# Kernel optimization log

Hardware: AMD Instinct MI355X
Metric: run time of the kernel (lower is better)

Reference implementation:

```python
import jax, jax.numpy as jnp
import numpy as np

H, DH = 8, 64            # heads, dim_head (module defaults)
B, N, DN, DE = 1, 512, 128, 64  # batch, nodes, node feat, edge feat
INNER = H * DH


def _w(key, fan_in, fan_out):
    return jax.random.normal(key, (fan_in, fan_out), jnp.float32) / np.sqrt(fan_in)


def setup_inputs() -> dict:
    key = jax.random.key(0)
    ks = jax.random.split(key, 8)
    return {
        "nodes": jax.random.normal(ks[0], (B, N, DN), jnp.float32),
        "edges": jax.random.normal(ks[1], (B, N, N, DE), jnp.float32),
        "mask": jnp.ones((B, N), dtype=bool),
        "Wq": _w(ks[2], DN, INNER), "bq": jnp.zeros((INNER,), jnp.float32),
        "Wk": _w(ks[3], DN, INNER), "bk": jnp.zeros((INNER,), jnp.float32),
        "Wv": _w(ks[4], DN, INNER), "bv": jnp.zeros((INNER,), jnp.float32),
        "We": _w(ks[5], DE, INNER), "be": jnp.zeros((INNER,), jnp.float32),
        "Wo": _w(ks[6], INNER, DN), "bo": jnp.zeros((DN,), jnp.float32),
    }


def _split_heads(x):
    # (b, ..., h*d) -> (b*h, ..., d), matching rearrange 'b ... (h d) -> (b h) ... d'
    b = x.shape[0]
    mid = x.shape[1:-1]
    x = x.reshape(b, *mid, H, DH)
    x = jnp.moveaxis(x, -2, 1)              # (b, h, ..., d)
    return x.reshape(b * H, *mid, DH)


def reference(nodes, edges, mask, Wq, bq, Wk, bk, Wv, bv, We, be, Wo, bo):
    scale = DH ** (-0.5)
    q = _split_heads(nodes @ Wq + bq)        # (bh, n, d)
    k = _split_heads(nodes @ Wk + bk)        # (bh, n, d)
    v = _split_heads(nodes @ Wv + bv)        # (bh, n, d)
    e = _split_heads(edges @ We + be)        # (bh, n, n, d) -- ek == ev == e_kv
    k = k[:, None, :, :] + e                 # (bh, i, j, d) per-ij keys
    v = v[:, None, :, :] + e                 # (bh, i, j, d) per-ij values
    sim = jnp.einsum('bid,bijd->bij', q, k) * scale
    m = mask[:, :, None] & mask[:, None, :]  # (b, i, j)
    m = jnp.repeat(m, H, axis=0)             # (bh, i, j)
    sim = jnp.where(m, sim, -jnp.finfo(sim.dtype).max)
    attn = jax.nn.softmax(sim, axis=-1)
    out = jnp.einsum('bij,bijd->bid', attn, v)           # (bh, n, d)
    out = out.reshape(B, H, N, DH).transpose(0, 2, 1, 3).reshape(B, N, INNER)
    return out @ Wo + bo                                  # (b, n, d_node)
```

## Files before the change

kernel.cpp:

```cpp
#include <hip/hip_runtime.h>
#include <hip/hip_bf16.h>

#define NN 512
#define DNODE 128
#define DEDGE 64
#define NH 8
#define DHD 64
#define DIN 512
#define SCALE 0.125f
#define ESTR 66

typedef unsigned short u16;
typedef unsigned int u32;

__device__ __forceinline__ float bf2f(u16 b) {
    u32 u = ((u32)b) << 16;
    return __builtin_bit_cast(float, u);
}
__device__ __forceinline__ u16 f2bf(float f) {
    u32 u = __builtin_bit_cast(u32, f);
    return (u16)((u + 0x7fffu + ((u >> 16) & 1u)) >> 16);
}

__global__ __launch_bounds__(256) void k_qkv(
    const float* __restrict__ nodes,
    const float* __restrict__ Wq, const float* __restrict__ bq,
    const float* __restrict__ Wk, const float* __restrict__ bk,
    const float* __restrict__ Wv, const float* __restrict__ bv,
    float* __restrict__ Qo, float* __restrict__ Ko, float* __restrict__ Vo)
{
    const int it = blockIdx.x, ct = blockIdx.y, which = blockIdx.z;
    const float* W    = which == 0 ? Wq : (which == 1 ? Wk : Wv);
    const float* bias = which == 0 ? bq : (which == 1 ? bk : bv);
    float* O          = which == 0 ? Qo : (which == 1 ? Ko : Vo);
    __shared__ float As[64][132];
    __shared__ float Bs[128][68];
    const int t = threadIdx.x;
    const int ibase = it * 64, cbase = ct * 64;
#pragma unroll
    for (int p = 0; p < 8; ++p) {
        int r = p * 8 + (t >> 5), c4 = (t & 31) * 4;
        *(float4*)&As[r][c4] = *(const float4*)(nodes + (ibase + r) * DNODE + c4);
    }
#pragma unroll
    for (int p = 0; p < 8; ++p) {
        int k = p * 16 + (t >> 4), c4 = (t & 15) * 4;
        *(float4*)&Bs[k][c4] = *(const float4*)(W + k * DIN + cbase + c4);
    }
    __syncthreads();
    const int tx = t & 15, ty = t >> 4;
    float acc[4][4] = {};
    for (int k = 0; k < DNODE; ++k) {
        float4 b4 = *(const float4*)&Bs[k][tx * 4];
#pragma unroll
        for (int e = 0; e < 4; ++e) {
            float a = As[ty * 4 + e][k];
            acc[e][0] += a * b4.x; acc[e][1] += a * b4.y;
            acc[e][2] += a * b4.z; acc[e][3] += a * b4.w;
        }
    }
    const int h = ct;
#pragma unroll
    for (int ii = 0; ii < 4; ++ii) {
        int i = ibase + ty * 4 + ii;
        float4 o;
        o.x = acc[ii][0] + bias[cbase + tx * 4 + 0];
        o.y = acc[ii][1] + bias[cbase + tx * 4 + 1];
        o.z = acc[ii][2] + bias[cbase + tx * 4 + 2];
        o.w = acc[ii][3] + bias[cbase + tx * 4 + 3];
        *(float4*)(O + ((size_t)h * NN + i) * DHD + tx * 4) = o;
    }
}

__global__ __launch_bounds__(256) void k_qe(
    const float* __restrict__ Q, const float* __restrict__ We, float* __restrict__ QE)
{
    const int it = blockIdx.x, h = blockIdx.y;
    __shared__ float Qs[64][68];
    __shared__ float WsT[64][68];
    const int t = threadIdx.x;
    const int ibase = it * 64;
#pragma unroll
    for (int p = 0; p < 4; ++p) {
        int r = p * 16 + (t >> 4), d4 = (t & 15) * 4;
        *(float4*)&Qs[r][d4] = *(const float4*)(Q + ((size_t)h * NN + ibase + r) * DHD + d4);
    }
#pragma unroll
    for (int p = 0; p < 4; ++p) {
        int c = p * 16 + (t >> 4), d4 = (t & 15) * 4;
        float4 v = *(const float4*)(We + c * DIN + h * DHD + d4);
        WsT[d4 + 0][c] = v.x; WsT[d4 + 1][c] = v.y;
        WsT[d4 + 2][c] = v.z; WsT[d4 + 3][c] = v.w;
    }
    __syncthreads();
    const int tx = t & 15, ty = t >> 4;
    float acc[4][4] = {};
    for (int d = 0; d < DHD; ++d) {
        float4 b4 = *(const float4*)&WsT[d][tx * 4];
#pragma unroll
        for (int e = 0; e < 4; ++e) {
            float a = Qs[ty * 4 + e][d];
            acc[e][0] += a * b4.x; acc[e][1] += a * b4.y;
            acc[e][2] += a * b4.z; acc[e][3] += a * b4.w;
        }
    }
#pragma unroll
    for (int ii = 0; ii < 4; ++ii) {
        int i = ibase + ty * 4 + ii;
        float4 o;
        o.x = SCALE * acc[ii][0]; o.y = SCALE * acc[ii][1];
        o.z = SCALE * acc[ii][2]; o.w = SCALE * acc[ii][3];
        *(float4*)(QE + ((size_t)h * NN + i) * DEDGE + tx * 4) = o;
    }
}

__global__ __launch_bounds__(256) void k_qk(
    const float* __restrict__ Q, const float* __restrict__ K, float* __restrict__ QK)
{
    const int jt = blockIdx.x, it = blockIdx.y, h = blockIdx.z;
    __shared__ float Qs[64][68];
    __shared__ float KsT[64][68];
    const int t = threadIdx.x;
    const int ibase = it * 64, jbase = jt * 64;
#pragma unroll
    for (int p = 0; p < 4; ++p) {
        int r = p * 16 + (t >> 4), d4 = (t & 15) * 4;
        *(float4*)&Qs[r][d4] = *(const float4*)(Q + ((size_t)h * NN + ibase + r) * DHD + d4);
    }
#pragma unroll
    for (int p = 0; p < 4; ++p) {
        int j = p * 16 + (t >> 4), d4 = (t & 15) * 4;
        float4 v = *(const float4*)(K + ((size_t)h * NN + jbase + j) * DHD + d4);
        KsT[d4 + 0][j] = v.x; KsT[d4 + 1][j] = v.y;
        KsT[d4 + 2][j] = v.z; KsT[d4 + 3][j] = v.w;
    }
    __syncthreads();
    const int tx = t & 15, ty = t >> 4;
    float acc[4][4] = {};
    for (int d = 0; d < DHD; ++d) {
        float4 b4 = *(const float4*)&KsT[d][tx * 4];
#pragma unroll
        for (int e = 0; e < 4; ++e) {
            float a = Qs[ty * 4 + e][d];
            acc[e][0] += a * b4.x; acc[e][1] += a * b4.y;
            acc[e][2] += a * b4.z; acc[e][3] += a * b4.w;
        }
    }
#pragma unroll
    for (int ii = 0; ii < 4; ++ii) {
        int i = ibase + ty * 4 + ii;
        float4 o;
        o.x = SCALE * acc[ii][0]; o.y = SCALE * acc[ii][1];
        o.z = SCALE * acc[ii][2]; o.w = SCALE * acc[ii][3];
        *(float4*)(QK + ((size_t)h * NN + i) * NN + jbase + tx * 4) = o;
    }
}

__global__ __launch_bounds__(512, 2) void k_fused(
    const float* __restrict__ edges, const float* __restrict__ QK,
    const float* __restrict__ QE, float* __restrict__ AE, u16* __restrict__ P)
{
    __shared__ u16 erow[NN * ESTR];
    __shared__ u16 Pl[NH][NN];
    __shared__ float qes[NH][DEDGE];
    const int i = blockIdx.x;
    const int t = threadIdx.x;
    const int lane = t & 63, w = t >> 6;

    qes[w][lane] = QE[((size_t)w * NN + i) * DEDGE + lane];

    const float* E = edges + (size_t)i * NN * DEDGE;
#pragma unroll
    for (int p = 0; p < 16; ++p) {
        int idx = p * 2048 + t * 4;
        float4 v = *(const float4*)(E + idx);
        int j = idx >> 6, c = idx & 63;
        u16* dst = &erow[j * ESTR + c];
        *(u32*)(dst)     = ((u32)f2bf(v.x)) | (((u32)f2bf(v.y)) << 16);
        *(u32*)(dst + 2) = ((u32)f2bf(v.z)) | (((u32)f2bf(v.w)) << 16);
    }
    __syncthreads();

    float sim[8];
    const float* qk = QK + ((size_t)w * NN + i) * NN;
#pragma unroll
    for (int r = 0; r < 8; ++r) {
        int j = r * 64 + lane;
        const u16* er = erow + j * ESTR;
        float acc = 0.f;
#pragma unroll
        for (int c = 0; c < 64; c += 4) {
            float4 q4 = *(const float4*)&qes[w][c];
            u32 lo = *(const u32*)(er + c);
            u32 hi = *(const u32*)(er + c + 2);
            acc += q4.x * bf2f((u16)(lo & 0xffff)) + q4.y * bf2f((u16)(lo >> 16))
                 + q4.z * bf2f((u16)(hi & 0xffff)) + q4.w * bf2f((u16)(hi >> 16));
        }
        sim[r] = qk[j] + acc;
    }

    float m = sim[0];
#pragma unroll
    for (int r = 1; r < 8; ++r) m = fmaxf(m, sim[r]);
#pragma unroll
    for (int s = 32; s >= 1; s >>= 1) m = fmaxf(m, __shfl_xor(m, s, 64));
    float p[8], l = 0.f;
#pragma unroll
    for (int r = 0; r < 8; ++r) { p[r] = __expf(sim[r] - m); l += p[r]; }
#pragma unroll
    for (int s = 32; s >= 1; s >>= 1) l += __shfl_xor(l, s, 64);
    float inv = 1.f / l;
    u16* Pg = P + ((size_t)w * NN + i) * NN;
#pragma unroll
    for (int r = 0; r < 8; ++r) {
        u16 pb = f2bf(p[r] * inv);
        Pl[w][r * 64 + lane] = pb;
        Pg[r * 64 + lane] = pb;
    }
    __syncthreads();

    float ae0 = 0.f, ae1 = 0.f, ae2 = 0.f, ae3 = 0.f;
    const u16* ec = erow + lane;
    for (int j0 = 0; j0 < NN; j0 += 8) {
        uint4 pk = *(const uint4*)&Pl[w][j0];
        const u16* e0 = ec + j0 * ESTR;
        ae0 += bf2f((u16)(pk.x & 0xffff)) * bf2f(e0[0 * ESTR]);
        ae1 += bf2f((u16)(pk.x >> 16))    * bf2f(e0[1 * ESTR]);
        ae2 += bf2f((u16)(pk.y & 0xffff)) * bf2f(e0[2 * ESTR]);
        ae3 += bf2f((u16)(pk.y >> 16))    * bf2f(e0[3 * ESTR]);
        ae0 += bf2f((u16)(pk.z & 0xffff)) * bf2f(e0[4 * ESTR]);
        ae1 += bf2f((u16)(pk.z >> 16))    * bf2f(e0[5 * ESTR]);
        ae2 += bf2f((u16)(pk.w & 0xffff)) * bf2f(e0[6 * ESTR]);
        ae3 += bf2f((u16)(pk.w >> 16))    * bf2f(e0[7 * ESTR]);
    }
    AE[((size_t)w * NN + i) * DEDGE + lane] = ae0 + ae1 + ae2 + ae3;
}

__global__ __launch_bounds__(256) void k_pv(
    const u16* __restrict__ P, const float* __restrict__ V, float* __restrict__ OUTV)
{
    const int ks = blockIdx.x, it = blockIdx.y, h = blockIdx.z;
    __shared__ u16 Ps[64][136];
    __shared__ float Vs[128][68];
    const int t = threadIdx.x;
    const int ibase = it * 64, kbase = ks * 128;
#pragma unroll
    for (int p = 0; p < 4; ++p) {
        int r = p * 16 + (t >> 4), j8 = (t & 15) * 8;
        *(uint4*)&Ps[r][j8] = *(const uint4*)(P + ((size_t)h * NN + ibase + r) * NN + kbase + j8);
    }
#pragma unroll
    for (int p = 0; p < 8; ++p) {
        int j = p * 16 + (t >> 4), d4 = (t & 15) * 4;
        *(float4*)&Vs[j][d4] = *(const float4*)(V + ((size_t)h * NN + kbase + j) * DHD + d4);
    }
    __syncthreads();
    const int tx = t & 15, ty = t >> 4;
    float acc[4][4] = {};
    for (int k = 0; k < 128; ++k) {
        float4 b4 = *(const float4*)&Vs[k][tx * 4];
#pragma unroll
        for (int e = 0; e < 4; ++e) {
            float a = bf2f(Ps[ty * 4 + e][k]);
            acc[e][0] += a * b4.x; acc[e][1] += a * b4.y;
            acc[e][2] += a * b4.z; acc[e][3] += a * b4.w;
        }
    }
#pragma unroll
    for (int ii = 0; ii < 4; ++ii)
#pragma unroll
        for (int jj = 0; jj < 4; ++jj)
            unsafeAtomicAdd(&OUTV[((size_t)h * NN + ibase + ty * 4 + ii) * DHD + tx * 4 + jj],
                            acc[ii][jj]);
}

__global__ __launch_bounds__(256) void k_inner(
    const float* __restrict__ AE, const float* __restrict__ We, const float* __restrict__ be,
    const float* __restrict__ OUTV, float* __restrict__ INNER)
{
    const int it = blockIdx.x, h = blockIdx.y;
    __shared__ float AEs[64][68];
    __shared__ float Ws[64][68];
    const int t = threadIdx.x;
    const int ibase = it * 64;
#pragma unroll
    for (int p = 0; p < 4; ++p) {
        int r = p * 16 + (t >> 4), c4 = (t & 15) * 4;
        *(float4*)&AEs[r][c4] = *(const float4*)(AE + ((size_t)h * NN + ibase + r) * DEDGE + c4);
    }
#pragma unroll
    for (int p = 0; p < 4; ++p) {
        int c = p * 16 + (t >> 4), d4 = (t & 15) * 4;
        *(float4*)&Ws[c][d4] = *(const float4*)(We + c * DIN + h * DHD + d4);
    }
    __syncthreads();
    const int tx = t & 15, ty = t >> 4;
    float acc[4][4] = {};
    for (int c = 0; c < DEDGE; ++c) {
        float4 b4 = *(const float4*)&Ws[c][tx * 4];
#pragma unroll
        for (int e = 0; e < 4; ++e) {
            float a = AEs[ty * 4 + e][c];
            acc[e][0] += a * b4.x; acc[e][1] += a * b4.y;
            acc[e][2] += a * b4.z; acc[e][3] += a * b4.w;
        }
    }
#pragma unroll
    for (int ii = 0; ii < 4; ++ii) {
        int i = ibase + ty * 4 + ii;
        float4 ov = *(const float4*)(OUTV + ((size_t)h * NN + i) * DHD + tx * 4);
        float4 o;
        o.x = acc[ii][0] + ov.x + be[h * DHD + tx * 4 + 0];
        o.y = acc[ii][1] + ov.y + be[h * DHD + tx * 4 + 1];
        o.z = acc[ii][2] + ov.z + be[h * DHD + tx * 4 + 2];
        o.w = acc[ii][3] + ov.w + be[h * DHD + tx * 4 + 3];
        *(float4*)(INNER + (size_t)i * DIN + h * DHD + tx * 4) = o;
    }
}

__global__ __launch_bounds__(256) void k_out(
    const float* __restrict__ INNER, const float* __restrict__ Wo, const float* __restrict__ bo,
    float* __restrict__ out)
{
    const int ks = blockIdx.x, it = blockIdx.y;
    __shared__ float Is[64][68];
    __shared__ float Wos[64][136];
    const int t = threadIdx.x;
    const int ibase = it * 64, kbase = ks * 64;
#pragma unroll
    for (int p = 0; p < 4; ++p) {
        int r = p * 16 + (t >> 4), c4 = (t & 15) * 4;
        *(float4*)&Is[r][c4] = *(const float4*)(INNER + (size_t)(ibase + r) * DIN + kbase + c4);
    }
#pragma unroll
    for (int p = 0; p < 8; ++p) {
        int k = p * 8 + (t >> 5), n4 = (t & 31) * 4;
        *(float4*)&Wos[k][n4] = *(const float4*)(Wo + (size_t)(kbase + k) * DNODE + n4);
    }
    __syncthreads();
    const int tx = t & 15, ty = t >> 4;
    float acc[4][8] = {};
    for (int k = 0; k < 64; ++k) {
        float4 b0 = *(const float4*)&Wos[k][tx * 8];
        float4 b1 = *(const float4*)&Wos[k][tx * 8 + 4];
#pragma unroll
        for (int e = 0; e < 4; ++e) {
            float a = Is[ty * 4 + e][k];
            acc[e][0] += a * b0.x; acc[e][1] += a * b0.y;
            acc[e][2] += a * b0.z; acc[e][3] += a * b0.w;
            acc[e][4] += a * b1.x; acc[e][5] += a * b1.y;
            acc[e][6] += a * b1.z; acc[e][7] += a * b1.w;
        }
    }
#pragma unroll
    for (int ii = 0; ii < 4; ++ii)
#pragma unroll
        for (int nn = 0; nn < 8; ++nn) {
            float v = acc[ii][nn] + (ks == 0 ? bo[tx * 8 + nn] : 0.f);
            unsafeAtomicAdd(&out[(size_t)(ibase + ty * 4 + ii) * DNODE + tx * 8 + nn], v);
        }
}

extern "C" void kernel_launch(void* const* d_in, const int* in_sizes, int n_in,
                              void* d_out, int out_size, void* d_ws, size_t ws_size,
                              hipStream_t stream) {
    (void)in_sizes; (void)n_in; (void)out_size; (void)ws_size;
    const float* nodes = (const float*)d_in[0];
    const float* edges = (const float*)d_in[1];
    const float* Wq = (const float*)d_in[3];  const float* bq = (const float*)d_in[4];
    const float* Wk = (const float*)d_in[5];  const float* bk = (const float*)d_in[6];
    const float* Wv = (const float*)d_in[7];  const float* bv = (const float*)d_in[8];
    const float* We = (const float*)d_in[9];  const float* be = (const float*)d_in[10];
    const float* Wo = (const float*)d_in[11]; const float* bo = (const float*)d_in[12];
    float* out = (float*)d_out;

    float* ws    = (float*)d_ws;
    float* Qb    = ws;
    float* Kb    = Qb    + NH * NN * DHD;
    float* Vb    = Kb    + NH * NN * DHD;
    float* QEb   = Vb    + NH * NN * DHD;
    float* AEb   = QEb   + NH * NN * DHD;
    float* OUTVb = AEb   + NH * NN * DHD;
    float* INb   = OUTVb + NH * NN * DHD;
    float* QKb   = INb   + (size_t)NN * DIN;
    u16*   Pb    = (u16*)(QKb + (size_t)NH * NN * NN);

    hipMemsetAsync(OUTVb, 0, (size_t)NH * NN * DHD * sizeof(float), stream);
    hipMemsetAsync(out, 0, (size_t)NN * DNODE * sizeof(float), stream);

    k_qkv<<<dim3(8, 8, 3), 256, 0, stream>>>(nodes, Wq, bq, Wk, bk, Wv, bv, Qb, Kb, Vb);
    k_qe<<<dim3(8, 8), 256, 0, stream>>>(Qb, We, QEb);
    k_qk<<<dim3(8, 8, 8), 256, 0, stream>>>(Qb, Kb, QKb);
    k_fused<<<dim3(512), 512, 0, stream>>>(edges, QKb, QEb, AEb, Pb);
    k_pv<<<dim3(4, 8, 8), 256, 0, stream>>>(Pb, Vb, OUTVb);
    k_inner<<<dim3(8, 8), 256, 0, stream>>>(AEb, We, be, OUTVb, INb);
    k_out<<<dim3(8, 8), 256, 0, stream>>>(INb, Wo, bo, out);
}
```

Baseline: 213.9 us.

## Restructure fused edge kernel with swizzled LDS and per-column head reuse

Replaces the padded edge-row LDS layout with an XOR-swizzled 128-byte row layout, so both the row-wise QE·E reads and the column-wise P·E reads can use wide loads without bank conflicts. The P·E accumulation is reorganised so each thread owns a column pair and a j-range and computes all 8 heads from one edge load, combining partial sums with LDS atomics. It also prefetches the QK row into registers before the edge load and asks for 4 blocks per CU instead of 2. The risks are register pressure under the tighter launch bound and contention on the shared atomics.

Result: slower. 224.0 us (+4.7%).

```diff
diff --git a/kernel.cpp b/kernel.cpp
--- a/kernel.cpp
+++ b/kernel.cpp
@@ -8,7 +8,6 @@
 #define DHD 64
 #define DIN 512
 #define SCALE 0.125f
-#define ESTR 66
 
 typedef unsigned short u16;
 typedef unsigned int u32;
@@ -21,6 +20,8 @@
     u32 u = __builtin_bit_cast(u32, f);
     return (u16)((u + 0x7fffu + ((u >> 16) & 1u)) >> 16);
 }
+__device__ __forceinline__ float bflo(u32 u) { return __builtin_bit_cast(float, u << 16); }
+__device__ __forceinline__ float bfhi(u32 u) { return __builtin_bit_cast(float, u & 0xffff0000u); }
 
 __global__ __launch_bounds__(256) void k_qkv(
     const float* __restrict__ nodes,
@@ -156,47 +157,60 @@
     }
 }
 
-__global__ __launch_bounds__(512, 2) void k_fused(
+__global__ __launch_bounds__(512, 4) void k_fused(
     const float* __restrict__ edges, const float* __restrict__ QK,
     const float* __restrict__ QE, float* __restrict__ AE, u16* __restrict__ P)
 {
-    __shared__ u16 erow[NN * ESTR];
-    __shared__ u16 Pl[NH][NN];
+    __shared__ u16 erow[NN * 64];
+    __shared__ u16 PlT[NH * 520];
     __shared__ float qes[NH][DEDGE];
+    __shared__ float ae_acc[NH][DEDGE];
     const int i = blockIdx.x;
     const int t = threadIdx.x;
     const int lane = t & 63, w = t >> 6;
 
+    const float* qk = QK + ((size_t)w * NN + i) * NN;
+    float qkr[8];
+#pragma unroll
+    for (int r = 0; r < 8; ++r) qkr[r] = qk[r * 64 + lane];
     qes[w][lane] = QE[((size_t)w * NN + i) * DEDGE + lane];
+    ((float*)ae_acc)[t] = 0.f;
 
     const float* E = edges + (size_t)i * NN * DEDGE;
 #pragma unroll
-    for (int p = 0; p < 16; ++p) {
-        int idx = p * 2048 + t * 4;
-        float4 v = *(const float4*)(E + idx);
-        int j = idx >> 6, c = idx & 63;
-        u16* dst = &erow[j * ESTR + c];
-        *(u32*)(dst)     = ((u32)f2bf(v.x)) | (((u32)f2bf(v.y)) << 16);
-        *(u32*)(dst + 2) = ((u32)f2bf(v.z)) | (((u32)f2bf(v.w)) << 16);
+    for (int p = 0; p < 8; ++p) {
+        int j = p * 64 + (t >> 3);
+        int c0 = (t & 7) * 8;
+        const float* s = E + j * 64 + c0;
+        float4 a = *(const float4*)s;
+        float4 b = *(const float4*)(s + 4);
+        uint4 pk;
+        pk.x = (u32)f2bf(a.x) | ((u32)f2bf(a.y) << 16);
+        pk.y = (u32)f2bf(a.z) | ((u32)f2bf(a.w) << 16);
+        pk.z = (u32)f2bf(b.x) | ((u32)f2bf(b.y) << 16);
+        pk.w = (u32)f2bf(b.z) | ((u32)f2bf(b.w) << 16);
+        int sb = (j * 128 + c0 * 2) ^ ((j & 7) << 4);
+        *(uint4*)((char*)erow + sb) = pk;
     }
     __syncthreads();
 
     float sim[8];
-    const float* qk = QK + ((size_t)w * NN + i) * NN;
-#pragma unroll
-    for (int r = 0; r < 8; ++r) {
-        int j = r * 64 + lane;
-        const u16* er = erow + j * ESTR;
-        float acc = 0.f;
-#pragma unroll
-        for (int c = 0; c < 64; c += 4) {
-            float4 q4 = *(const float4*)&qes[w][c];
-            u32 lo = *(const u32*)(er + c);
-            u32 hi = *(const u32*)(er + c + 2);
-            acc += q4.x * bf2f((u16)(lo & 0xffff)) + q4.y * bf2f((u16)(lo >> 16))
-                 + q4.z * bf2f((u16)(hi & 0xffff)) + q4.w * bf2f((u16)(hi >> 16));
-        }
-        sim[r] = qk[j] + acc;
+#pragma unroll
+    for (int r = 0; r < 8; ++r) sim[r] = qkr[r];
+#pragma unroll
+    for (int cb = 0; cb < 8; ++cb) {
+        float4 qA = *(const float4*)&qes[w][cb * 8];
+        float4 qB = *(const float4*)&qes[w][cb * 8 + 4];
+#pragma unroll
+        for (int r = 0; r < 8; ++r) {
+            int j = r * 64 + lane;
+            uint4 ev = *(const uint4*)((const char*)erow +
+                        ((j * 128 + cb * 16) ^ ((j & 7) << 4)));
+            sim[r] += qA.x * bflo(ev.x) + qA.y * bfhi(ev.x)
+                    + qA.z * bflo(ev.y) + qA.w * bfhi(ev.y)
+                    + qB.x * bflo(ev.z) + qB.y * bfhi(ev.z)
+                    + qB.z * bflo(ev.w) + qB.w * bfhi(ev.w);
+        }
     }
 
     float m = sim[0];
@@ -204,36 +218,53 @@
     for (int r = 1; r < 8; ++r) m = fmaxf(m, sim[r]);
 #pragma unroll
     for (int s = 32; s >= 1; s >>= 1) m = fmaxf(m, __shfl_xor(m, s, 64));
-    float p[8], l = 0.f;
-#pragma unroll
-    for (int r = 0; r < 8; ++r) { p[r] = __expf(sim[r] - m); l += p[r]; }
+    float pr[8], l = 0.f;
+#pragma unroll
+    for (int r = 0; r < 8; ++r) { pr[r] = __expf(sim[r] - m); l += pr[r]; }
 #pragma unroll
     for (int s = 32; s >= 1; s >>= 1) l += __shfl_xor(l, s, 64);
     float inv = 1.f / l;
     u16* Pg = P + ((size_t)w * NN + i) * NN;
 #pragma unroll
     for (int r = 0; r < 8; ++r) {
-        u16 pb = f2bf(p[r] * inv);
-        Pl[w][r * 64 + lane] = pb;
+        u16 pb = f2bf(pr[r] * inv);
+        PlT[w * 520 + r * 64 + lane] = pb;
         Pg[r * 64 + lane] = pb;
     }
     __syncthreads();
 
-    float ae0 = 0.f, ae1 = 0.f, ae2 = 0.f, ae3 = 0.f;
-    const u16* ec = erow + lane;
-    for (int j0 = 0; j0 < NN; j0 += 8) {
-        uint4 pk = *(const uint4*)&Pl[w][j0];
-        const u16* e0 = ec + j0 * ESTR;
-        ae0 += bf2f((u16)(pk.x & 0xffff)) * bf2f(e0[0 * ESTR]);
-        ae1 += bf2f((u16)(pk.x >> 16))    * bf2f(e0[1 * ESTR]);
-        ae2 += bf2f((u16)(pk.y & 0xffff)) * bf2f(e0[2 * ESTR]);
-        ae3 += bf2f((u16)(pk.y >> 16))    * bf2f(e0[3 * ESTR]);
-        ae0 += bf2f((u16)(pk.z & 0xffff)) * bf2f(e0[4 * ESTR]);
-        ae1 += bf2f((u16)(pk.z >> 16))    * bf2f(e0[5 * ESTR]);
-        ae2 += bf2f((u16)(pk.w & 0xffff)) * bf2f(e0[6 * ESTR]);
-        ae3 += bf2f((u16)(pk.w >> 16))    * bf2f(e0[7 * ESTR]);
-    }
-    AE[((size_t)w * NN + i) * DEDGE + lane] = ae0 + ae1 + ae2 + ae3;
+    const int cp = lane & 31, jh = lane >> 5;
+    const int jbase = w * 64 + jh * 32;
+    float ae0[8] = {}, ae1[8] = {};
+#pragma unroll
+    for (int jb = 0; jb < 4; ++jb) {
+        int j0 = jbase + jb * 8;
+        float elo[8], ehi[8];
+#pragma unroll
+        for (int k = 0; k < 8; ++k) {
+            int j = j0 + k;
+            u32 ew = *(const u32*)((const char*)erow +
+                      ((j * 128 + cp * 4) ^ ((j & 7) << 4)));
+            elo[k] = bflo(ew); ehi[k] = bfhi(ew);
+        }
+#pragma unroll
+        for (int h = 0; h < 8; ++h) {
+            uint4 pv = *(const uint4*)&PlT[h * 520 + j0];
+            float p0 = bflo(pv.x), p1 = bfhi(pv.x), p2 = bflo(pv.y), p3 = bfhi(pv.y);
+            float p4 = bflo(pv.z), p5 = bfhi(pv.z), p6 = bflo(pv.w), p7 = bfhi(pv.w);
+            ae0[h] += p0 * elo[0] + p1 * elo[1] + p2 * elo[2] + p3 * elo[3]
+                    + p4 * elo[4] + p5 * elo[5] + p6 * elo[6] + p7 * elo[7];
+            ae1[h] += p0 * ehi[0] + p1 * ehi[1] + p2 * ehi[2] + p3 * ehi[3]
+                    + p4 * ehi[4] + p5 * ehi[5] + p6 * ehi[6] + p7 * ehi[7];
+        }
+    }
+#pragma unroll
+    for (int h = 0; h < 8; ++h) {
+        atomicAdd(&ae_acc[h][2 * cp],     ae0[h]);
+        atomicAdd(&ae_acc[h][2 * cp + 1], ae1[h]);
+    }
+    __syncthreads();
+    AE[(((size_t)(t >> 6)) * NN + i) * DEDGE + (t & 63)] = ((const float*)ae_acc)[t];
 }
 
 __global__ __launch_bounds__(256) void k_pv(
```
